# Kernel optimization log

Measured on AMD Instinct MI355X. Metric: run time of the kernel, lower is better.

Reference implementation:

```python
import jax, jax.numpy as jnp
import numpy as np

N = 150000      # hits in one event
K = 192         # max truth objects; t_idx in [-1, K-1], -1 = noise
C = 3           # n_ccoords
ENERGY_W = 1.0  # energy_loss_weight
POS_W = 1.0     # position_loss_weight
Q_MIN = 0.5
S_B = 1.0


def setup_inputs() -> dict:
    key = jax.random.key(0)
    ks = jax.random.split(key, 12)
    pred_beta = jax.random.uniform(ks[0], (N, 1), jnp.float32, 0.01, 0.99)
    pred_ccoords = jax.random.normal(ks[1], (N, C), jnp.float32)
    pred_energy = jax.random.uniform(ks[2], (N, 1), jnp.float32) * 50.0 + 1.0
    pred_pos = jax.random.normal(ks[3], (N, 2), jnp.float32) * 50.0 + 100.0
    pred_time = jax.random.normal(ks[4], (N, 1), jnp.float32)
    pred_id = jax.random.normal(ks[5], (N, 8), jnp.float32)
    # truth index: -1 = noise hit, 0..K-1 = object id
    t_idx = jax.random.randint(ks[6], (N, 1), 0, K + 1, jnp.int32) - 1
    t_energy = jax.random.uniform(ks[7], (N, 1), jnp.float32) * 50.0 + 1.0
    t_pos = jax.random.normal(ks[8], (N, 2), jnp.float32) * 50.0 + 100.0
    t_time = jax.random.uniform(ks[9], (N, 1), jnp.float32) + 0.5  # also used as energy weights
    t_pid = jax.random.randint(ks[10], (N, 1), 0, 6, jnp.int32)
    rowsplits = jnp.array([0, N], dtype=jnp.int32)  # single event
    return dict(pred_beta=pred_beta, pred_ccoords=pred_ccoords, pred_energy=pred_energy,
                pred_pos=pred_pos, pred_time=pred_time, pred_id=pred_id, t_idx=t_idx,
                t_energy=t_energy, t_pos=t_pos, t_time=t_time, t_pid=t_pid,
                rowsplits=rowsplits)


def _oc_loss(x, beta_in, tidx, energyweights, payload):
    """Object condensation potentials (single event, dense [N,K] formulation).
    x: [N,C] cluster coords, beta_in: [N], tidx: [N] (-1 noise), payload: [N,P]."""
    dt = x.dtype
    beta = jnp.clip(beta_in, 1e-4, 1.0 - 1e-4)
    q = (jnp.arctanh(beta) ** 2 + Q_MIN) * energyweights           # [N] charge

    M = tidx[:, None] == jnp.arange(K, dtype=tidx.dtype)[None, :]  # [N,K] membership
    Mf = M.astype(dt)
    obj_exists = jnp.any(M, axis=0)                                # [K]

    # condensation point alpha_k = argmax beta among hits of object k
    beta_masked = jnp.where(M, beta[:, None], -1.0)                # [N,K]
    alpha = jnp.argmax(beta_masked, axis=0)                        # [K]
    x_alpha = x[alpha]                                             # [K,C]
    q_alpha = q[alpha]                                             # [K]
    beta_alpha = beta[alpha]                                       # [K]

    d2 = jnp.sum((x[:, None, :] - x_alpha[None, :, :]) ** 2, axis=-1)  # [N,K]
    qq = (q[:, None] * q_alpha[None, :]) * obj_exists[None, :].astype(dt)

    n = jnp.asarray(x.shape[0], dt)
    att = jnp.sum(Mf * d2 * qq) / n                                    # attractive
    rep = jnp.sum((1.0 - Mf) * jnp.maximum(0.0, 1.0 - jnp.sqrt(d2 + 1e-9)) * qq) / n

    is_noise = tidx < 0
    n_noise = jnp.maximum(jnp.sum(is_noise.astype(dt)), 1.0)
    noise = S_B * jnp.sum(jnp.where(is_noise, beta, 0.0)) / n_noise

    n_obj = jnp.maximum(jnp.sum(obj_exists.astype(dt)), 1.0)
    min_b = jnp.sum(jnp.where(obj_exists, 1.0 - beta_alpha, 0.0)) / n_obj

    # payload: per-object beta-weighted mean, averaged over objects
    w = jnp.arctanh(beta) ** 2                                     # [N]
    wM = w[:, None] * Mf                                           # [N,K]
    wsum = jnp.sum(wM, axis=0) + 1e-9                              # [K]
    pay_k = (wM.T @ payload) / wsum[:, None]                       # [K,P]
    pay = jnp.sum(jnp.where(obj_exists[:, None], pay_k, 0.0), axis=0) / n_obj  # [P]

    exceed_beta = jnp.asarray(0.0, dt)  # too_much_beta_scale = 0
    return att, rep, noise, min_b, pay, exceed_beta


def reference(pred_beta, pred_ccoords, pred_energy, pred_pos, pred_time, pred_id,
              t_idx, t_energy, t_pos, t_time, t_pid, rowsplits):
    # payload losses (per hit)
    energy_loss = ENERGY_W * (t_energy - pred_energy) ** 2 / t_energy ** 2        # [N,1]
    position_loss = POS_W * jnp.sum((t_pos - pred_pos) ** 2 / t_pos ** 2,
                                    axis=-1, keepdims=True)                        # [N,1]
    full_payload = jnp.concatenate([energy_loss, position_loss], axis=-1)          # [N,2]

    energyweights = t_time[:, 0]  # note: source assigns energy_weights = t_time
    att, rep, noise, min_b, pay, exceed_beta = _oc_loss(
        pred_ccoords, pred_beta[:, 0], t_idx[:, 0], energyweights, full_payload)

    lossval = att + rep + min_b + noise + pay[0] + pay[1] + exceed_beta
    return lossval
```

## Files before the change

kernel.cpp:

```cpp
#include <hip/hip_runtime.h>

#define NPTS   150000
#define KOBJ   192
#define PBLK   256
#define PREP_T 512
#define NREP   8
#define MAIN_B 586

__device__ __forceinline__ float clipb(float b) {
    return fminf(fmaxf(b, 1e-4f), 1.0f - 1e-4f);
}

#define OFF_REPW (KOBJ * PBLK * 8)
#define OFF_REPP (OFF_REPW + NREP * KOBJ * 4)
#define OFF_SCAL (OFF_REPP + NREP * KOBJ * 4)
#define OFF_TICK (OFF_SCAL + 64)
#define OFF_XAQ  (OFF_TICK + 16)

__global__ __launch_bounds__(PREP_T) void k_prep(
        const float* __restrict__ pred_beta,
        const float* __restrict__ pred_energy,
        const float* __restrict__ pred_pos,
        const int*   __restrict__ t_idx,
        const float* __restrict__ t_energy,
        const float* __restrict__ t_pos,
        unsigned long long* __restrict__ pKey,
        float* __restrict__ repW,
        float* __restrict__ repP,
        float* __restrict__ scal) {
    __shared__ unsigned sBits[KOBJ], sIdx[KOBJ];
    __shared__ float sW[KOBJ], sP[KOBJ];
    __shared__ float sNs[PREP_T / 64], sNc[PREP_T / 64];
    const int tid = threadIdx.x;
    if (tid < KOBJ) { sBits[tid] = 0u; sIdx[tid] = 0xFFFFFFFFu; sW[tid] = 0.f; sP[tid] = 0.f; }
    __syncthreads();

    float nS = 0.f, nC = 0.f;
    const int i0 = blockIdx.x * PREP_T + tid;
    for (int i = i0; i < NPTS; i += PBLK * PREP_T) {
        const float b = clipb(pred_beta[i]);
        const int   t = t_idx[i];
        if (t >= 0) {
            atomicMax(&sBits[t], __float_as_uint(b));
            const float a = atanhf(b);
            const float w = a * a;
            const float pe = pred_energy[i], te = t_energy[i];
            const float el = (te - pe) * (te - pe) / (te * te);
            const float pp0 = pred_pos[2 * i],  pp1 = pred_pos[2 * i + 1];
            const float tp0 = t_pos[2 * i],     tp1 = t_pos[2 * i + 1];
            const float pl = (tp0 - pp0) * (tp0 - pp0) / (tp0 * tp0)
                           + (tp1 - pp1) * (tp1 - pp1) / (tp1 * tp1);
            atomicAdd(&sW[t], w);
            atomicAdd(&sP[t], w * (el + pl));
        } else {
            nS += b; nC += 1.f;
        }
    }
    __syncthreads();
    for (int i = i0; i < NPTS; i += PBLK * PREP_T) {
        const int t = t_idx[i];
        if (t >= 0 && __float_as_uint(clipb(pred_beta[i])) == sBits[t])
            atomicMin(&sIdx[t], (unsigned)i);
    }
    for (int off = 32; off > 0; off >>= 1) {
        nS += __shfl_down(nS, off);
        nC += __shfl_down(nC, off);
    }
    if ((tid & 63) == 0) { sNs[tid >> 6] = nS; sNc[tid >> 6] = nC; }
    __syncthreads();

    if (tid < KOBJ) {
        const unsigned long long key =
            ((unsigned long long)sBits[tid] << 32) |
            (unsigned long long)(0xFFFFFFFFu - sIdx[tid]);
        pKey[(size_t)tid * PBLK + blockIdx.x] = key;
        const float w = sW[tid];
        if (w != 0.f) {
            const int r = (blockIdx.x & (NREP - 1)) * KOBJ + tid;
            atomicAdd(&repW[r], w);
            atomicAdd(&repP[r], sP[tid]);
        }
    }
    if (tid == 0) {
        float s = 0.f, c = 0.f;
        for (int w = 0; w < PREP_T / 64; ++w) { s += sNs[w]; c += sNc[w]; }
        if (c != 0.f) { atomicAdd(&scal[2], s); atomicAdd(&scal[3], c); }
    }
}

__global__ __launch_bounds__(64) void k_objs(
        const float* __restrict__ pred_beta,
        const float* __restrict__ pred_ccoords,
        const float* __restrict__ t_time,
        const unsigned long long* __restrict__ pKey,
        const float* __restrict__ repW,
        const float* __restrict__ repP,
        float4* __restrict__ xaq,
        float* __restrict__ scal) {
    const int k = blockIdx.x, lane = threadIdx.x;
    const unsigned long long* row = pKey + (size_t)k * PBLK;
    unsigned long long best = 0ULL;
    #pragma unroll
    for (int p = lane; p < PBLK; p += 64) {
        const unsigned long long v = row[p];
        if (v > best) best = v;
    }
    float w = 0.f, pay = 0.f;
    if (lane < NREP) { w = repW[lane * KOBJ + k]; pay = repP[lane * KOBJ + k]; }
    for (int off = 32; off > 0; off >>= 1) {
        const unsigned long long ob = __shfl_down(best, off);
        if (ob > best) best = ob;
        w   += __shfl_down(w,   off);
        pay += __shfl_down(pay, off);
    }
    if (lane == 0) {
        float4 v = make_float4(0.f, 0.f, 0.f, 0.f);
        if (best != 0ULL) {
            const unsigned ai = 0xFFFFFFFFu - (unsigned)(best & 0xFFFFFFFFull);
            const float b = clipb(pred_beta[ai]);
            const float a = atanhf(b);
            v.x = pred_ccoords[3 * ai];
            v.y = pred_ccoords[3 * ai + 1];
            v.z = pred_ccoords[3 * ai + 2];
            v.w = (a * a + 0.5f) * t_time[ai];
            atomicAdd(&scal[4], 1.0f - b);
            atomicAdd(&scal[5], pay / (w + 1e-9f));
            atomicAdd(&scal[6], 1.0f);
        }
        xaq[k] = v;
    }
}

__device__ __forceinline__ float rep_term(float x0, float x1, float x2,
                                          float a0, float a1, float a2, float qw) {
    const float d0 = x0 - a0, d1 = x1 - a1, d2 = x2 - a2;
    const float dd = d0 * d0 + d1 * d1 + d2 * d2 + 1e-9f;
    return fmaxf(1.0f - __builtin_amdgcn_sqrtf(dd), 0.f) * qw;
}

__global__ __launch_bounds__(256) void k_main(
        const float* __restrict__ pred_beta,
        const float* __restrict__ pred_ccoords,
        const int*   __restrict__ t_idx,
        const float* __restrict__ t_time,
        const float4* __restrict__ xaq,
        float* __restrict__ scal,
        unsigned int* __restrict__ tick,
        float* __restrict__ out) {
    __shared__ float s0[KOBJ], s1[KOBJ], s2[KOBJ], sq[KOBJ];
    const int tid = threadIdx.x;
    if (tid < KOBJ) {
        const float4 v = xaq[tid];
        s0[tid] = v.x; s1[tid] = v.y; s2[tid] = v.z; sq[tid] = v.w;
    }
    __syncthreads();

    const int i = blockIdx.x * 256 + tid;
    float rep = 0.f, att = 0.f;
    if (i < NPTS) {
        const float x0 = pred_ccoords[3 * i];
        const float x1 = pred_ccoords[3 * i + 1];
        const float x2 = pred_ccoords[3 * i + 2];
        const float b  = clipb(pred_beta[i]);
        const float a  = atanhf(b);
        const float q  = (a * a + 0.5f) * t_time[i];
        const int own  = t_idx[i];

        float r0 = 0.f, r1 = 0.f, r2 = 0.f, r3 = 0.f;
        #pragma unroll 4
        for (int kk = 0; kk < KOBJ; kk += 4) {
            r0 += rep_term(x0, x1, x2, s0[kk],     s1[kk],     s2[kk],     sq[kk]);
            r1 += rep_term(x0, x1, x2, s0[kk + 1], s1[kk + 1], s2[kk + 1], sq[kk + 1]);
            r2 += rep_term(x0, x1, x2, s0[kk + 2], s1[kk + 2], s2[kk + 2], sq[kk + 2]);
            r3 += rep_term(x0, x1, x2, s0[kk + 3], s1[kk + 3], s2[kk + 3], sq[kk + 3]);
        }
        rep = (r0 + r1) + (r2 + r3);
        if (own >= 0) {
            const float d0 = x0 - s0[own], d1 = x1 - s1[own], d2 = x2 - s2[own];
            const float dd = d0 * d0 + d1 * d1 + d2 * d2;
            rep -= fmaxf(1.0f - __builtin_amdgcn_sqrtf(dd + 1e-9f), 0.f) * sq[own];
            att  = dd * sq[own];
        }
        rep *= q; att *= q;
    }

    for (int off = 32; off > 0; off >>= 1) {
        rep += __shfl_down(rep, off);
        att += __shfl_down(att, off);
    }
    __shared__ float wr[4], wa[4];
    const int wid = tid >> 6, lane = tid & 63;
    if (lane == 0) { wr[wid] = rep; wa[wid] = att; }
    __syncthreads();
    if (tid == 0) {
        atomicAdd(&scal[0], wa[0] + wa[1] + wa[2] + wa[3]);
        atomicAdd(&scal[1], wr[0] + wr[1] + wr[2] + wr[3]);
        __threadfence();
        const unsigned old = atomicAdd(tick, 1u);
        if (old == MAIN_B - 1) {
            const float attS = atomicAdd(&scal[0], 0.f);
            const float repS = atomicAdd(&scal[1], 0.f);
            const float nS   = atomicAdd(&scal[2], 0.f);
            const float nC   = atomicAdd(&scal[3], 0.f);
            const float mbS  = atomicAdd(&scal[4], 0.f);
            const float payS = atomicAdd(&scal[5], 0.f);
            const float cnt  = atomicAdd(&scal[6], 0.f);
            const float n    = (float)NPTS;
            const float nobj = fmaxf(cnt, 1.0f);
            out[0] = attS / n + repS / n + nS / fmaxf(nC, 1.0f)
                   + mbS / nobj + payS / nobj;
        }
    }
}

extern "C" void kernel_launch(void* const* d_in, const int* in_sizes, int n_in,
                              void* d_out, int out_size, void* d_ws, size_t ws_size,
                              hipStream_t stream) {
    const float* pred_beta    = (const float*)d_in[0];
    const float* pred_ccoords = (const float*)d_in[1];
    const float* pred_energy  = (const float*)d_in[2];
    const float* pred_pos     = (const float*)d_in[3];
    const int*   t_idx        = (const int*)  d_in[6];
    const float* t_energy     = (const float*)d_in[7];
    const float* t_pos        = (const float*)d_in[8];
    const float* t_time       = (const float*)d_in[9];

    char* ws = (char*)d_ws;
    unsigned long long* pKey = (unsigned long long*)ws;
    float*        repW = (float*)(ws + OFF_REPW);
    float*        repP = (float*)(ws + OFF_REPP);
    float*        scal = (float*)(ws + OFF_SCAL);
    unsigned int* tick = (unsigned int*)(ws + OFF_TICK);
    float4*       xaq  = (float4*)(ws + OFF_XAQ);

    hipMemsetAsync(ws + OFF_REPW, 0, OFF_XAQ - OFF_REPW, stream);

    k_prep<<<PBLK, PREP_T, 0, stream>>>(pred_beta, pred_energy, pred_pos,
                                        t_idx, t_energy, t_pos,
                                        pKey, repW, repP, scal);
    k_objs<<<KOBJ, 64, 0, stream>>>(pred_beta, pred_ccoords, t_time,
                                    pKey, repW, repP, xaq, scal);
    k_main<<<MAIN_B, 256, 0, stream>>>(pred_beta, pred_ccoords, t_idx, t_time,
                                       xaq, scal, tick, (float*)d_out);
}
```

Measured before the change: 131.1 us.

## Split main kernel over object halves and replace atomics with partial arrays

The main repulsion kernel now launches twice as many blocks, each covering half of the 192 objects, which raises parallelism across the GPU. All global float atomics and the memset are removed. Per-block partials are written to workspace arrays, and the last block reduces them. The tick counter is reset inside k_prep instead of by a memset. In exchange, each hit's coordinates and beta are loaded and atanh is computed twice, and the final block does a larger serial reduction.

```diff
diff --git a/kernel.cpp b/kernel.cpp
--- a/kernel.cpp
+++ b/kernel.cpp
@@ -1,21 +1,28 @@
 #include <hip/hip_runtime.h>
 
-#define NPTS   150000
-#define KOBJ   192
-#define PBLK   256
-#define PREP_T 512
-#define NREP   8
-#define MAIN_B 586
+#define NPTS    150000
+#define KOBJ    192
+#define PBLK    256
+#define PREP_T  512
+#define MAIN_PB 586
+#define KH      96
+#define MAIN_GRID (MAIN_PB * 2)
 
 __device__ __forceinline__ float clipb(float b) {
     return fminf(fmaxf(b, 1e-4f), 1.0f - 1e-4f);
 }
 
-#define OFF_REPW (KOBJ * PBLK * 8)
-#define OFF_REPP (OFF_REPW + NREP * KOBJ * 4)
-#define OFF_SCAL (OFF_REPP + NREP * KOBJ * 4)
-#define OFF_TICK (OFF_SCAL + 64)
-#define OFF_XAQ  (OFF_TICK + 16)
+#define OFF_PW   (KOBJ * PBLK * 8)
+#define OFF_PP   (OFF_PW  + KOBJ * PBLK * 4)
+#define OFF_NZS  (OFF_PP  + KOBJ * PBLK * 4)
+#define OFF_NZC  (OFF_NZS + PBLK * 4)
+#define OFF_MB   (OFF_NZC + PBLK * 4)
+#define OFF_PAY  (OFF_MB  + KOBJ * 4)
+#define OFF_EX   (OFF_PAY + KOBJ * 4)
+#define OFF_XAQ  (OFF_EX  + KOBJ * 4)
+#define OFF_ATTP (OFF_XAQ + KOBJ * 16)
+#define OFF_REPP (OFF_ATTP + MAIN_GRID * 4)
+#define OFF_TICK (OFF_REPP + MAIN_GRID * 4)
 
 __global__ __launch_bounds__(PREP_T) void k_prep(
         const float* __restrict__ pred_beta,
@@ -25,9 +32,11 @@
         const float* __restrict__ t_energy,
         const float* __restrict__ t_pos,
         unsigned long long* __restrict__ pKey,
-        float* __restrict__ repW,
-        float* __restrict__ repP,
-        float* __restrict__ scal) {
+        float* __restrict__ pW,
+        float* __restrict__ pP,
+        float* __restrict__ nzS,
+        float* __restrict__ nzC,
+        unsigned int* __restrict__ tick) {
     __shared__ unsigned sBits[KOBJ], sIdx[KOBJ];
     __shared__ float sW[KOBJ], sP[KOBJ];
     __shared__ float sNs[PREP_T / 64], sNc[PREP_T / 64];
@@ -73,18 +82,17 @@
         const unsigned long long key =
             ((unsigned long long)sBits[tid] << 32) |
             (unsigned long long)(0xFFFFFFFFu - sIdx[tid]);
-        pKey[(size_t)tid * PBLK + blockIdx.x] = key;
-        const float w = sW[tid];
-        if (w != 0.f) {
-            const int r = (blockIdx.x & (NREP - 1)) * KOBJ + tid;
-            atomicAdd(&repW[r], w);
-            atomicAdd(&repP[r], sP[tid]);
-        }
+        const size_t o = (size_t)tid * PBLK + blockIdx.x;
+        pKey[o] = key;
+        pW[o]   = sW[tid];
+        pP[o]   = sP[tid];
     }
     if (tid == 0) {
         float s = 0.f, c = 0.f;
         for (int w = 0; w < PREP_T / 64; ++w) { s += sNs[w]; c += sNc[w]; }
-        if (c != 0.f) { atomicAdd(&scal[2], s); atomicAdd(&scal[3], c); }
+        nzS[blockIdx.x] = s;
+        nzC[blockIdx.x] = c;
+        *tick = 0u;
     }
 }
 
@@ -93,20 +101,23 @@
         const float* __restrict__ pred_ccoords,
         const float* __restrict__ t_time,
         const unsigned long long* __restrict__ pKey,
-        const float* __restrict__ repW,
-        const float* __restrict__ repP,
+        const float* __restrict__ pW,
+        const float* __restrict__ pP,
         float4* __restrict__ xaq,
-        float* __restrict__ scal) {
+        float* __restrict__ mbA,
+        float* __restrict__ payA,
+        float* __restrict__ exA) {
     const int k = blockIdx.x, lane = threadIdx.x;
-    const unsigned long long* row = pKey + (size_t)k * PBLK;
+    const size_t row = (size_t)k * PBLK;
     unsigned long long best = 0ULL;
+    float w = 0.f, pay = 0.f;
     #pragma unroll
     for (int p = lane; p < PBLK; p += 64) {
-        const unsigned long long v = row[p];
+        const unsigned long long v = pKey[row + p];
         if (v > best) best = v;
-    }
-    float w = 0.f, pay = 0.f;
-    if (lane < NREP) { w = repW[lane * KOBJ + k]; pay = repP[lane * KOBJ + k]; }
+        w   += pW[row + p];
+        pay += pP[row + p];
+    }
     for (int off = 32; off > 0; off >>= 1) {
         const unsigned long long ob = __shfl_down(best, off);
         if (ob > best) best = ob;
@@ -115,6 +126,7 @@
     }
     if (lane == 0) {
         float4 v = make_float4(0.f, 0.f, 0.f, 0.f);
+        float mb = 0.f, pk = 0.f, ex = 0.f;
         if (best != 0ULL) {
             const unsigned ai = 0xFFFFFFFFu - (unsigned)(best & 0xFFFFFFFFull);
             const float b = clipb(pred_beta[ai]);
@@ -123,11 +135,11 @@
             v.y = pred_ccoords[3 * ai + 1];
             v.z = pred_ccoords[3 * ai + 2];
             v.w = (a * a + 0.5f) * t_time[ai];
-            atomicAdd(&scal[4], 1.0f - b);
-            atomicAdd(&scal[5], pay / (w + 1e-9f));
-            atomicAdd(&scal[6], 1.0f);
-        }
-        xaq[k] = v;
+            mb = 1.0f - b;
+            pk = pay / (w + 1e-9f);
+            ex = 1.f;
+        }
+        xaq[k] = v; mbA[k] = mb; payA[k] = pk; exA[k] = ex;
     }
 }
 
@@ -136,6 +148,15 @@
     const float d0 = x0 - a0, d1 = x1 - a1, d2 = x2 - a2;
     const float dd = d0 * d0 + d1 * d1 + d2 * d2 + 1e-9f;
     return fmaxf(1.0f - __builtin_amdgcn_sqrtf(dd), 0.f) * qw;
+}
+
+__device__ __forceinline__ float block_sum(float v, float* red, int tid) {
+    for (int off = 32; off > 0; off >>= 1) v += __shfl_down(v, off);
+    if ((tid & 63) == 0) red[tid >> 6] = v;
+    __syncthreads();
+    const float r = red[0] + red[1] + red[2] + red[3];
+    __syncthreads();
+    return r;
 }
 
 __global__ __launch_bounds__(256) void k_main(
@@ -144,18 +165,27 @@
         const int*   __restrict__ t_idx,
         const float* __restrict__ t_time,
         const float4* __restrict__ xaq,
-        float* __restrict__ scal,
+        const float* __restrict__ nzS,
+        const float* __restrict__ nzC,
+        const float* __restrict__ mbA,
+        const float* __restrict__ payA,
+        const float* __restrict__ exA,
+        float* __restrict__ attP,
+        float* __restrict__ repP,
         unsigned int* __restrict__ tick,
         float* __restrict__ out) {
-    __shared__ float s0[KOBJ], s1[KOBJ], s2[KOBJ], sq[KOBJ];
+    __shared__ float s0[KH], s1[KH], s2[KH], sq[KH];
+    __shared__ float red[4];
+    __shared__ int sLast;
     const int tid = threadIdx.x;
-    if (tid < KOBJ) {
-        const float4 v = xaq[tid];
+    const int k0  = (blockIdx.x & 1) * KH;
+    if (tid < KH) {
+        const float4 v = xaq[k0 + tid];
         s0[tid] = v.x; s1[tid] = v.y; s2[tid] = v.z; sq[tid] = v.w;
     }
     __syncthreads();
 
-    const int i = blockIdx.x * 256 + tid;
+    const int i = (blockIdx.x >> 1) * 256 + tid;
     float rep = 0.f, att = 0.f;
     if (i < NPTS) {
         const float x0 = pred_ccoords[3 * i];
@@ -164,22 +194,22 @@
         const float b  = clipb(pred_beta[i]);
         const float a  = atanhf(b);
         const float q  = (a * a + 0.5f) * t_time[i];
-        const int own  = t_idx[i];
+        const int oj   = t_idx[i] - k0;
 
         float r0 = 0.f, r1 = 0.f, r2 = 0.f, r3 = 0.f;
         #pragma unroll 4
-        for (int kk = 0; kk < KOBJ; kk += 4) {
+        for (int kk = 0; kk < KH; kk += 4) {
             r0 += rep_term(x0, x1, x2, s0[kk],     s1[kk],     s2[kk],     sq[kk]);
             r1 += rep_term(x0, x1, x2, s0[kk + 1], s1[kk + 1], s2[kk + 1], sq[kk + 1]);
             r2 += rep_term(x0, x1, x2, s0[kk + 2], s1[kk + 2], s2[kk + 2], sq[kk + 2]);
             r3 += rep_term(x0, x1, x2, s0[kk + 3], s1[kk + 3], s2[kk + 3], sq[kk + 3]);
         }
         rep = (r0 + r1) + (r2 + r3);
-        if (own >= 0) {
-            const float d0 = x0 - s0[own], d1 = x1 - s1[own], d2 = x2 - s2[own];
+        if (oj >= 0 && oj < KH) {
+            const float d0 = x0 - s0[oj], d1 = x1 - s1[oj], d2 = x2 - s2[oj];
             const float dd = d0 * d0 + d1 * d1 + d2 * d2;
-            rep -= fmaxf(1.0f - __builtin_amdgcn_sqrtf(dd + 1e-9f), 0.f) * sq[own];
-            att  = dd * sq[own];
+            rep -= fmaxf(1.0f - __builtin_amdgcn_sqrtf(dd + 1e-9f), 0.f) * sq[oj];
+            att  = dd * sq[oj];
         }
         rep *= q; att *= q;
     }
@@ -189,25 +219,39 @@
         att += __shfl_down(att, off);
     }
     __shared__ float wr[4], wa[4];
-    const int wid = tid >> 6, lane = tid & 63;
-    if (lane == 0) { wr[wid] = rep; wa[wid] = att; }
+    const int wid = tid >> 6;
+    if ((tid & 63) == 0) { wr[wid] = rep; wa[wid] = att; }
     __syncthreads();
     if (tid == 0) {
-        atomicAdd(&scal[0], wa[0] + wa[1] + wa[2] + wa[3]);
-        atomicAdd(&scal[1], wr[0] + wr[1] + wr[2] + wr[3]);
+        attP[blockIdx.x] = wa[0] + wa[1] + wa[2] + wa[3];
+        repP[blockIdx.x] = wr[0] + wr[1] + wr[2] + wr[3];
         __threadfence();
         const unsigned old = atomicAdd(tick, 1u);
-        if (old == MAIN_B - 1) {
-            const float attS = atomicAdd(&scal[0], 0.f);
-            const float repS = atomicAdd(&scal[1], 0.f);
-            const float nS   = atomicAdd(&scal[2], 0.f);
-            const float nC   = atomicAdd(&scal[3], 0.f);
-            const float mbS  = atomicAdd(&scal[4], 0.f);
-            const float payS = atomicAdd(&scal[5], 0.f);
-            const float cnt  = atomicAdd(&scal[6], 0.f);
+        sLast = (old == MAIN_GRID - 1) ? 1 : 0;
+    }
+    __syncthreads();
+    if (sLast) {
+        float aS = 0.f, rS = 0.f;
+        for (int b = tid; b < MAIN_GRID; b += 256) {
+            aS += atomicAdd(&attP[b], 0.f);
+            rS += atomicAdd(&repP[b], 0.f);
+        }
+        float mb = 0.f, pay = 0.f, ex = 0.f;
+        if (tid < KOBJ) { mb = mbA[tid]; pay = payA[tid]; ex = exA[tid]; }
+        const float ns = nzS[tid];
+        const float nc = nzC[tid];
+
+        const float attS = block_sum(aS, red, tid);
+        const float repS = block_sum(rS, red, tid);
+        const float mbS  = block_sum(mb, red, tid);
+        const float payS = block_sum(pay, red, tid);
+        const float exS  = block_sum(ex, red, tid);
+        const float nSs  = block_sum(ns, red, tid);
+        const float nCs  = block_sum(nc, red, tid);
+        if (tid == 0) {
             const float n    = (float)NPTS;
-            const float nobj = fmaxf(cnt, 1.0f);
-            out[0] = attS / n + repS / n + nS / fmaxf(nC, 1.0f)
+            const float nobj = fmaxf(exS, 1.0f);
+            out[0] = attS / n + repS / n + nSs / fmaxf(nCs, 1.0f)
                    + mbS / nobj + payS / nobj;
         }
     }
@@ -227,19 +271,24 @@
 
     char* ws = (char*)d_ws;
     unsigned long long* pKey = (unsigned long long*)ws;
-    float*        repW = (float*)(ws + OFF_REPW);
+    float*        pW   = (float*)(ws + OFF_PW);
+    float*        pP   = (float*)(ws + OFF_PP);
+    float*        nzS  = (float*)(ws + OFF_NZS);
+    float*        nzC  = (float*)(ws + OFF_NZC);
+    float*        mbA  = (float*)(ws + OFF_MB);
+    float*        payA = (float*)(ws + OFF_PAY);
+    float*        exA  = (float*)(ws + OFF_EX);
+    float4*       xaq  = (float4*)(ws + OFF_XAQ);
+    float*        attP = (float*)(ws + OFF_ATTP);
     float*        repP = (float*)(ws + OFF_REPP);
-    float*        scal = (float*)(ws + OFF_SCAL);
     unsigned int* tick = (unsigned int*)(ws + OFF_TICK);
-    float4*       xaq  = (float4*)(ws + OFF_XAQ);
-
-    hipMemsetAsync(ws + OFF_REPW, 0, OFF_XAQ - OFF_REPW, stream);
 
     k_prep<<<PBLK, PREP_T, 0, stream>>>(pred_beta, pred_energy, pred_pos,
                                         t_idx, t_energy, t_pos,
-                                        pKey, repW, repP, scal);
+                                        pKey, pW, pP, nzS, nzC, tick);
     k_objs<<<KOBJ, 64, 0, stream>>>(pred_beta, pred_ccoords, t_time,
-                                    pKey, repW, repP, xaq, scal);
-    k_main<<<MAIN_B, 256, 0, stream>>>(pred_beta, pred_ccoords, t_idx, t_time,
-                                       xaq, scal, tick, (float*)d_out);
-}
+                                    pKey, pW, pP, xaq, mbA, payA, exA);
+    k_main<<<MAIN_GRID, 256, 0, stream>>>(pred_beta, pred_ccoords, t_idx, t_time,
+                                          xaq, nzS, nzC, mbA, payA, exA,
+                                          attP, repP, tick, (float*)d_out);
+}
```

Result: faster. 120.2 us (-8.3%).
